# Kernel optimization log

Measured on AMD Instinct MI355X. Metric: run time of the kernel, lower is better.

## Reference

```python
import jax, jax.numpy as jnp
import numpy as np

D_MODEL = 1024
D_QK = 1024
NUM_HEADS = 16
HEAD_DIM = D_QK // NUM_HEADS      # 64
V_DIM = D_MODEL // NUM_HEADS      # 64
B, S = 2, 2048


def setup_inputs() -> dict:
    key = jax.random.key(0)
    ks = jax.random.split(key, 9)
    sc = 0.02
    return {
        "x": jax.random.normal(ks[0], (B, S, D_MODEL), dtype=jnp.float32),
        "Wqk": jax.random.normal(ks[1], (D_MODEL, 2 * D_QK), dtype=jnp.float32) * sc,
        "bqk": jax.random.normal(ks[2], (2 * D_QK,), dtype=jnp.float32) * sc,
        "Wv": jax.random.normal(ks[3], (D_MODEL, D_MODEL), dtype=jnp.float32) * sc,
        "bv": jax.random.normal(ks[4], (D_MODEL,), dtype=jnp.float32) * sc,
        "Wn": jax.random.normal(ks[5], (D_MODEL, NUM_HEADS), dtype=jnp.float32) * sc,
        "bn": jax.random.normal(ks[6], (NUM_HEADS,), dtype=jnp.float32) * sc,
        "Wo": jax.random.normal(ks[7], (D_MODEL, D_MODEL), dtype=jnp.float32) * sc,
        "bo": jax.random.normal(ks[8], (D_MODEL,), dtype=jnp.float32) * sc,
    }


def reference(x, Wqk, bqk, Wv, bv, Wn, bn, Wo, bo):
    b, s, _ = x.shape
    qk = x @ Wqk + bqk                                  # (B,S,2*D_QK)
    v = x @ Wv + bv                                     # (B,S,D_MODEL)
    n = x @ Wn + bn                                     # (B,S,H)

    qk = qk.reshape(b, s, 2, NUM_HEADS, HEAD_DIM)
    q, k = qk[:, :, 0], qk[:, :, 1]                     # (B,S,H,Dh)
    v = v.reshape(b, s, NUM_HEADS, V_DIM)               # (B,S,H,Dv)

    scores = jnp.einsum('bthd,bshd->bhts', q, k)        # (B,H,S,S)
    mask = jnp.tril(jnp.ones((s, s), dtype=scores.dtype))
    n_exp = jnp.exp(jnp.transpose(n, (0, 2, 1)))        # (B,H,S)
    attn = scores * mask / n_exp[:, :, :, None]         # dropout p=0 (eval)

    ctx = jnp.einsum('bhts,bshd->bthd', attn, v)        # (B,S,H,Dv)
    ctx = ctx.reshape(b, s, D_MODEL)
    return ctx @ Wo + bo
```

## Files before the change

kernel.cpp:

```cpp
#include <hip/hip_runtime.h>
#include <hip/hip_bf16.h>

constexpr int Bb   = 2;
constexpr int Ss   = 2048;
constexpr int Dm   = 1024;
constexpr int Hh   = 16;
constexpr int Hd   = 64;
constexpr int Mtot = Bb * Ss;
constexpr int NCH  = Ss / 64;

typedef __bf16 bf16x8 __attribute__((ext_vector_type(8)));
typedef float  f32x4  __attribute__((ext_vector_type(4)));
typedef __attribute__((address_space(1))) unsigned int u32_as1;
typedef __attribute__((address_space(3))) unsigned int u32_as3;

__device__ __forceinline__ void gload_lds16(const void* g, void* l) {
  __builtin_amdgcn_global_load_lds((const u32_as1*)g, (u32_as3*)l, 16, 0, 0);
}

__device__ __forceinline__ unsigned short f2bf(float f) {
  union { float f; unsigned u; } x; x.f = f;
  unsigned r = x.u + 0x7fffu + ((x.u >> 16) & 1u);
  return (unsigned short)(r >> 16);
}

__device__ __forceinline__ float bf2f(unsigned short s) {
  union { unsigned u; float f; } x; x.u = ((unsigned)s) << 16;
  return x.f;
}

__global__ __launch_bounds__(256) void k_prep(
    const float* __restrict__ x, const float* __restrict__ Wn, const float* __restrict__ bn,
    float* __restrict__ invn, unsigned short* __restrict__ xb,
    const float* __restrict__ Wqk, const float* __restrict__ Wv, const float* __restrict__ Wo,
    unsigned short* __restrict__ wprojT, unsigned short* __restrict__ woT) {
  __shared__ __align__(16) char smem[16384];
  int bi = blockIdx.x;
  int tid = threadIdx.x;
  if (bi < 1024) {
    float (*xl)[1024] = (float(*)[1024])smem;
    int w = tid >> 6, lane = tid & 63;
    int row = bi * 4 + w;
    const float4* x4 = (const float4*)(x + (size_t)row * Dm);
    ushort4* xb4 = (ushort4*)(xb + (size_t)row * Dm);
#pragma unroll
    for (int j = 0; j < 4; ++j) {
      float4 v = x4[j * 64 + lane];
      *(float4*)&xl[w][(j * 64 + lane) * 4] = v;
      ushort4 o;
      o.x = f2bf(v.x); o.y = f2bf(v.y); o.z = f2bf(v.z); o.w = f2bf(v.w);
      xb4[j * 64 + lane] = o;
    }
    __syncthreads();
    const float4* Wn4 = (const float4*)Wn;
    f32x4 sum = {0.f, 0.f, 0.f, 0.f};
#pragma unroll 4
    for (int j = 0; j < 64; ++j) {
      float xv = xl[w][j * 16 + (lane >> 2)];
      float4 wv = Wn4[j * 64 + lane];
      sum[0] += xv * wv.x; sum[1] += xv * wv.y; sum[2] += xv * wv.z; sum[3] += xv * wv.w;
    }
#pragma unroll
    for (int m = 4; m < 64; m <<= 1) {
      sum[0] += __shfl_xor(sum[0], m);
      sum[1] += __shfl_xor(sum[1], m);
      sum[2] += __shfl_xor(sum[2], m);
      sum[3] += __shfl_xor(sum[3], m);
    }
    if (lane < 4) {
      int b = row >> 11, s = row & 2047;
#pragma unroll
      for (int e = 0; e < 4; ++e) {
        int h = lane * 4 + e;
        float nv = sum[e] + bn[h];
        invn[((size_t)(b * Hh + h)) * Ss + s] = expf(-nv);
      }
    }
  } else {
    float (*t)[33] = (float(*)[33])smem;
    int ti = bi - 1024;
    const float* W; unsigned short* Wt; int N, n0, k0;
    if (ti < 2048) {
      W = Wqk; Wt = wprojT; N = 2048;
      n0 = (ti & 63) * 32; k0 = (ti >> 6) * 32;
    } else if (ti < 3072) {
      int l = ti - 2048; W = Wv; Wt = wprojT + (size_t)2048 * 1024; N = 1024;
      n0 = (l & 31) * 32; k0 = (l >> 5) * 32;
    } else {
      int l = ti - 3072; W = Wo; Wt = woT; N = 1024;
      n0 = (l & 31) * 32; k0 = (l >> 5) * 32;
    }
    int tx = tid & 31, ty = tid >> 5;
#pragma unroll
    for (int j = 0; j < 32; j += 8)
      t[ty + j][tx] = W[(size_t)(k0 + ty + j) * N + n0 + tx];
    __syncthreads();
#pragma unroll
    for (int j = 0; j < 32; j += 8)
      Wt[(size_t)(n0 + ty + j) * 1024 + k0 + tx] = f2bf(t[tx][ty + j]);
  }
}

__global__ __launch_bounds__(256, 4) void k_gemm_proj(
    const unsigned short* __restrict__ A, const unsigned short* __restrict__ BT,
    const float* __restrict__ bias0, const float* __restrict__ bias1,
    void* __restrict__ out0, void* __restrict__ out1, void* __restrict__ out2,
    void* __restrict__ out3, int M, int N, int K) {
  __shared__ __align__(16) unsigned short As[128 * 64];
  __shared__ __align__(16) unsigned short Bs[128 * 64];
  int tid = threadIdx.x, w = tid >> 6, lane = tid & 63;
  int bid = blockIdx.y * gridDim.x + blockIdx.x;
  int xcd = bid & 7, idx = bid >> 3;
  int m0 = (xcd * 4 + (idx & 3)) * 128;
  int n0 = (idx >> 2) * 128;
  int wm = w >> 1, wn = w & 1;
  f32x4 acc[4][4] = {};

  for (int kt = 0; kt < (K >> 6); ++kt) {
#pragma unroll
    for (int i = 0; i < 4; ++i) {
      int lin = i * 2048 + w * 512 + lane * 8;
      int r = lin >> 6, c = lin & 63;
      gload_lds16(A + (size_t)(m0 + r) * K + kt * 64 + c, As + i * 2048 + w * 512);
    }
#pragma unroll
    for (int i = 0; i < 4; ++i) {
      int lin = i * 2048 + w * 512 + lane * 8;
      int r = lin >> 6, c = lin & 63;
      gload_lds16(BT + (size_t)(n0 + r) * K + kt * 64 + c, Bs + i * 2048 + w * 512);
    }
    __syncthreads();
#pragma unroll
    for (int ks = 0; ks < 2; ++ks) {
      bf16x8 af[4], bfr[4];
#pragma unroll
      for (int mt = 0; mt < 4; ++mt)
        af[mt] = *(const bf16x8*)(As + (wm * 64 + mt * 16 + (lane & 15)) * 64 + ks * 32 + (lane >> 4) * 8);
#pragma unroll
      for (int nt = 0; nt < 4; ++nt)
        bfr[nt] = *(const bf16x8*)(Bs + (wn * 64 + nt * 16 + (lane & 15)) * 64 + ks * 32 + (lane >> 4) * 8);
#pragma unroll
      for (int mt = 0; mt < 4; ++mt)
#pragma unroll
        for (int nt = 0; nt < 4; ++nt)
          acc[mt][nt] = __builtin_amdgcn_mfma_f32_16x16x32_bf16(af[mt], bfr[nt], acc[mt][nt], 0, 0, 0);
    }
    __syncthreads();
  }

#pragma unroll
  for (int mt = 0; mt < 4; ++mt) {
#pragma unroll
    for (int nt = 0; nt < 4; ++nt) {
      int n = n0 + wn * 64 + nt * 16 + (lane & 15);
      int tbase = m0 + wm * 64 + mt * 16 + (lane >> 4) * 4;
      int region = n >> 10;
      int h = (n >> 6) & 15, d = n & 63;
      int b = tbase >> 11, t = tbase & 2047;
      float bb = (region < 2) ? bias0[n] : bias1[n - 2048];
      if (region == 0) {
        unsigned short* qp = (unsigned short*)out0;
#pragma unroll
        for (int r = 0; r < 4; ++r)
          qp[(((size_t)(b * Hh + h)) * Ss + t + r) * Hd + d] = f2bf(acc[mt][nt][r] + bb);
      } else if (region == 1) {
        unsigned short* kp = (unsigned short*)out1;
#pragma unroll
        for (int r = 0; r < 4; ++r)
          kp[(((size_t)(b * Hh + h)) * Ss + t + r) * Hd + d] = f2bf(acc[mt][nt][r] + bb);
        ushort4 o;
        o.x = f2bf(acc[mt][nt][0] + bb);
        o.y = f2bf(acc[mt][nt][1] + bb);
        o.z = f2bf(acc[mt][nt][2] + bb);
        o.w = f2bf(acc[mt][nt][3] + bb);
        *(ushort4*)((unsigned short*)out2 + ((size_t)(b * Hh + h) * Hd + d) * Ss + t) = o;
      } else {
        ushort4 o;
        o.x = f2bf(acc[mt][nt][0] + bb);
        o.y = f2bf(acc[mt][nt][1] + bb);
        o.z = f2bf(acc[mt][nt][2] + bb);
        o.w = f2bf(acc[mt][nt][3] + bb);
        *(ushort4*)((unsigned short*)out3 + ((size_t)(b * Hh + h) * Hd + d) * Ss + t) = o;
      }
    }
  }
}

__global__ __launch_bounds__(256, 3) void k_gemm_o(
    const unsigned short* __restrict__ A, const unsigned short* __restrict__ BT,
    const float* __restrict__ bias, float* __restrict__ out) {
  constexpr int K = 1024, N = 1024;
  __shared__ __align__(16) unsigned short As[2][64 * 64];
  __shared__ __align__(16) unsigned short Bs[2][128 * 64];
  int tid = threadIdx.x, w = tid >> 6, lane = tid & 63;
  int bid = blockIdx.y * gridDim.x + blockIdx.x;
  int xcd = bid & 7, idx = bid >> 3;
  int m0 = (xcd * 8 + (idx & 7)) * 64;
  int n0 = (idx >> 3) * 128;
  int wm = w >> 1, wn = w & 1;
  f32x4 acc[2][4] = {};

  auto STAGE = [&](int kt, int cur) {
#pragma unroll
    for (int i = 0; i < 2; ++i) {
      int lin = i * 2048 + w * 512 + lane * 8;
      int r = lin >> 6, c = lin & 63;
      gload_lds16(A + (size_t)(m0 + r) * K + kt * 64 + c, As[cur] + i * 2048 + w * 512);
    }
#pragma unroll
    for (int i = 0; i < 4; ++i) {
      int lin = i * 2048 + w * 512 + lane * 8;
      int r = lin >> 6, c = lin & 63;
      gload_lds16(BT + (size_t)(n0 + r) * K + kt * 64 + c, Bs[cur] + i * 2048 + w * 512);
    }
  };

  constexpr int NT = K >> 6;
  STAGE(0, 0);
  __syncthreads();
  for (int kt = 0; kt < NT; ++kt) {
    int cur = kt & 1;
    if (kt + 1 < NT) STAGE(kt + 1, cur ^ 1);
#pragma unroll
    for (int ks = 0; ks < 2; ++ks) {
      bf16x8 af[2], bfr[4];
#pragma unroll
      for (int mt = 0; mt < 2; ++mt)
        af[mt] = *(const bf16x8*)(As[cur] + (wm * 32 + mt * 16 + (lane & 15)) * 64 + ks * 32 + (lane >> 4) * 8);
#pragma unroll
      for (int nt = 0; nt < 4; ++nt)
        bfr[nt] = *(const bf16x8*)(Bs[cur] + (wn * 64 + nt * 16 + (lane & 15)) * 64 + ks * 32 + (lane >> 4) * 8);
#pragma unroll
      for (int mt = 0; mt < 2; ++mt)
#pragma unroll
        for (int nt = 0; nt < 4; ++nt)
          acc[mt][nt] = __builtin_amdgcn_mfma_f32_16x16x32_bf16(af[mt], bfr[nt], acc[mt][nt], 0, 0, 0);
    }
    __syncthreads();
  }

#pragma unroll
  for (int mt = 0; mt < 2; ++mt) {
#pragma unroll
    for (int nt = 0; nt < 4; ++nt) {
      int n = n0 + wn * 64 + nt * 16 + (lane & 15);
      int m = m0 + wm * 32 + mt * 16 + (lane >> 4) * 4;
      float bb = bias[n];
#pragma unroll
      for (int r = 0; r < 4; ++r)
        out[(size_t)(m + r) * N + n] = acc[mt][nt][r] + bb;
    }
  }
}

__global__ __launch_bounds__(64) void k_gram(
    const unsigned short* __restrict__ vT, const unsigned short* __restrict__ kT,
    unsigned short* __restrict__ G) {
  int lane = threadIdx.x;
  int j = blockIdx.x, bh = blockIdx.y;
  int t0 = j * 64;
  const unsigned short* vb = vT + (size_t)bh * Hd * Ss;
  const unsigned short* kb = kT + (size_t)bh * Hd * Ss;
  unsigned short* g = G + ((size_t)bh * NCH + j) * 4096;

  bf16x8 af[4][2], bfr[4][2];
#pragma unroll
  for (int mt = 0; mt < 4; ++mt)
#pragma unroll
    for (int ks = 0; ks < 2; ++ks) {
      af[mt][ks]  = *(const bf16x8*)(vb + (size_t)(mt * 16 + (lane & 15)) * Ss + t0 + ks * 32 + (lane >> 4) * 8);
      bfr[mt][ks] = *(const bf16x8*)(kb + (size_t)(mt * 16 + (lane & 15)) * Ss + t0 + ks * 32 + (lane >> 4) * 8);
    }
  f32x4 acc[4][4] = {};
#pragma unroll
  for (int mt = 0; mt < 4; ++mt)
#pragma unroll
    for (int nt = 0; nt < 4; ++nt)
#pragma unroll
      for (int ks = 0; ks < 2; ++ks)
        acc[mt][nt] = __builtin_amdgcn_mfma_f32_16x16x32_bf16(af[mt][ks], bfr[nt][ks], acc[mt][nt], 0, 0, 0);
#pragma unroll
  for (int mt = 0; mt < 4; ++mt)
#pragma unroll
    for (int nt = 0; nt < 4; ++nt)
#pragma unroll
      for (int r = 0; r < 4; ++r)
        g[(mt * 16 + (lane >> 4) * 4 + r) * 64 + nt * 16 + (lane & 15)] = f2bf(acc[mt][nt][r]);
}

__global__ __launch_bounds__(256) void k_prefix(
    const unsigned short* __restrict__ G, unsigned short* __restrict__ Sp) {
  int gidx = blockIdx.x * 256 + threadIdx.x;
  int bh = gidx >> 12, e = gidx & 4095;
  const unsigned short* gp = G + (size_t)bh * NCH * 4096 + e;
  unsigned short* sp = Sp + (size_t)bh * NCH * 4096 + e;
  float acc = 0.f;
#pragma unroll 8
  for (int j = 0; j < NCH; ++j) {
    sp[(size_t)j * 4096] = f2bf(acc);
    acc += bf2f(gp[(size_t)j * 4096]);
  }
}

__global__ __launch_bounds__(256, 6) void k_chunk_attn(
    const unsigned short* __restrict__ q, const unsigned short* __restrict__ k,
    const unsigned short* __restrict__ vT, const unsigned short* __restrict__ Sp,
    const float* __restrict__ invn, unsigned short* __restrict__ ctx) {
  __shared__ __align__(16) unsigned short P[4 * 16 * 64];
  int tid = threadIdx.x, w = tid >> 6, lane = tid & 63;
  int j = blockIdx.x, bh = blockIdx.y;
  int t0 = j * 64;
  const unsigned short* qb = q + (size_t)bh * Ss * Hd;
  const unsigned short* kb = k + (size_t)bh * Ss * Hd;
  const unsigned short* vb = vT + (size_t)bh * Hd * Ss;
  const unsigned short* sp = Sp + ((size_t)bh * NCH + j) * 4096;

  bf16x8 qf[2];
#pragma unroll
  for (int ks = 0; ks < 2; ++ks)
    qf[ks] = *(const bf16x8*)(qb + (size_t)(t0 + w * 16 + (lane & 15)) * Hd + ks * 32 + (lane >> 4) * 8);

  f32x4 acc[4] = {};
#pragma unroll
  for (int nt = 0; nt < 4; ++nt)
#pragma unroll
    for (int ks = 0; ks < 2; ++ks) {
      bf16x8 sf = *(const bf16x8*)(sp + (nt * 16 + (lane & 15)) * 64 + ks * 32 + (lane >> 4) * 8);
      acc[nt] = __builtin_amdgcn_mfma_f32_16x16x32_bf16(qf[ks], sf, acc[nt], 0, 0, 0);
    }

  f32x4 sacc[4] = {};
#pragma unroll
  for (int nt = 0; nt < 4; ++nt)
#pragma unroll
    for (int ks = 0; ks < 2; ++ks) {
      bf16x8 kf = *(const bf16x8*)(kb + (size_t)(t0 + nt * 16 + (lane & 15)) * Hd + ks * 32 + (lane >> 4) * 8);
      sacc[nt] = __builtin_amdgcn_mfma_f32_16x16x32_bf16(qf[ks], kf, sacc[nt], 0, 0, 0);
    }

#pragma unroll
  for (int nt = 0; nt < 4; ++nt)
#pragma unroll
    for (int r = 0; r < 4; ++r) {
      int row = (lane >> 4) * 4 + r;
      int s_local = nt * 16 + (lane & 15);
      float vv = (s_local <= w * 16 + row) ? sacc[nt][r] : 0.f;
      int cb = s_local * 2;
      int byte = w * 2048 + row * 128 + (cb ^ ((row & 7) << 4));
      *(unsigned short*)((char*)P + byte) = f2bf(vv);
    }
  asm volatile("" ::: "memory");

  bf16x8 pf[2];
#pragma unroll
  for (int ks = 0; ks < 2; ++ks) {
    int prow = lane & 15;
    int pcb = (ks * 32 + (lane >> 4) * 8) * 2;
    pf[ks] = *(const bf16x8*)((char*)P + w * 2048 + prow * 128 + (pcb ^ ((prow & 7) << 4)));
  }
#pragma unroll
  for (int dt = 0; dt < 4; ++dt)
#pragma unroll
    for (int ks = 0; ks < 2; ++ks) {
      bf16x8 vf = *(const bf16x8*)(vb + (size_t)(dt * 16 + (lane & 15)) * Ss + t0 + ks * 32 + (lane >> 4) * 8);
      acc[dt] = __builtin_amdgcn_mfma_f32_16x16x32_bf16(pf[ks], vf, acc[dt], 0, 0, 0);
    }

  int b = bh >> 4, h = bh & 15;
  float sc[4];
#pragma unroll
  for (int r = 0; r < 4; ++r)
    sc[r] = invn[(size_t)bh * Ss + t0 + w * 16 + (lane >> 4) * 4 + r];
#pragma unroll
  for (int dt = 0; dt < 4; ++dt)
#pragma unroll
    for (int r = 0; r < 4; ++r) {
      int t = t0 + w * 16 + (lane >> 4) * 4 + r;
      size_t m = (size_t)b * Ss + t;
      ctx[m * Dm + h * Hd + dt * 16 + (lane & 15)] = f2bf(acc[dt][r] * sc[r]);
    }
}

extern "C" void kernel_launch(void* const* d_in, const int* in_sizes, int n_in,
                              void* d_out, int out_size, void* d_ws, size_t ws_size,
                              hipStream_t stream) {
  const float* x   = (const float*)d_in[0];
  const float* Wqk = (const float*)d_in[1];
  const float* bqk = (const float*)d_in[2];
  const float* Wv  = (const float*)d_in[3];
  const float* bv  = (const float*)d_in[4];
  const float* Wn  = (const float*)d_in[5];
  const float* bn  = (const float*)d_in[6];
  const float* Wo  = (const float*)d_in[7];
  const float* bo  = (const float*)d_in[8];

  char* ws = (char*)d_ws;
  size_t off = 0;
  unsigned short* xb    = (unsigned short*)(ws + off); off += (size_t)Mtot * Dm * 2;
  unsigned short* wprojT= (unsigned short*)(ws + off); off += (size_t)3072 * 1024 * 2;
  unsigned short* woT   = (unsigned short*)(ws + off); off += (size_t)1024 * 1024 * 2;
  unsigned short* qbuf  = (unsigned short*)(ws + off); off += (size_t)Bb * Hh * Ss * Hd * 2;
  unsigned short* kbuf  = (unsigned short*)(ws + off); off += (size_t)Bb * Hh * Ss * Hd * 2;
  unsigned short* ktbuf = (unsigned short*)(ws + off); off += (size_t)Bb * Hh * Ss * Hd * 2;
  unsigned short* vbuf  = (unsigned short*)(ws + off); off += (size_t)Bb * Hh * Ss * Hd * 2;
  float* invn           = (float*)(ws + off);          off += (size_t)Bb * Hh * Ss * 4;
  unsigned short* G     = (unsigned short*)(ws + off); off += (size_t)Bb * Hh * NCH * 4096 * 2;
  unsigned short* Sp    = (unsigned short*)(ws + off); off += (size_t)Bb * Hh * NCH * 4096 * 2;
  unsigned short* ctx   = xb;

  k_prep<<<5120, 256, 0, stream>>>(x, Wn, bn, invn, xb, Wqk, Wv, Wo, wprojT, woT);

  k_gemm_proj<<<dim3(3072 / 128, Mtot / 128), 256, 0, stream>>>(
      xb, wprojT, bqk, bv, qbuf, kbuf, ktbuf, vbuf, Mtot, 3072, 1024);

  k_gram<<<dim3(NCH, Bb * Hh), 64, 0, stream>>>(vbuf, ktbuf, G);
  k_prefix<<<(Bb * Hh * 4096) / 256, 256, 0, stream>>>(G, Sp);
  k_chunk_attn<<<dim3(NCH, Bb * Hh), 256, 0, stream>>>(qbuf, kbuf, vbuf, Sp, invn, ctx);

  k_gemm_o<<<dim3(1024 / 128, Mtot / 64), 256, 0, stream>>>(ctx, woT, bo, (float*)d_out);
}
```

Baseline: 104.0 us.

## Rewrite projection GEMM as 256x256 double-buffered 8-wave pipelined kernel

Replaces the 128x128, 256-thread projection GEMM with a 256x256 tile, 512-thread kernel. It double-buffers 128KB of LDS, issues the next k-step's global-to-LDS loads between MFMA groups, and XOR-swizzles the LDS columns to avoid bank conflicts. It also remaps blocks across XCDs and raises MFMA priority with setprio. The goal is to hide global load latency and improve operand reuse, at the cost of fewer, larger blocks (192) and heavier register and LDS pressure.

```diff
diff --git a/kernel.cpp b/kernel.cpp
--- a/kernel.cpp
+++ b/kernel.cpp
@@ -101,59 +101,100 @@
   }
 }
 
-__global__ __launch_bounds__(256, 4) void k_gemm_proj(
+__global__ __launch_bounds__(512, 2) void k_gemm_proj8(
     const unsigned short* __restrict__ A, const unsigned short* __restrict__ BT,
     const float* __restrict__ bias0, const float* __restrict__ bias1,
     void* __restrict__ out0, void* __restrict__ out1, void* __restrict__ out2,
-    void* __restrict__ out3, int M, int N, int K) {
-  __shared__ __align__(16) unsigned short As[128 * 64];
-  __shared__ __align__(16) unsigned short Bs[128 * 64];
+    void* __restrict__ out3) {
+  constexpr int K = 1024, NT = 16;
+  __shared__ __align__(16) char lds[131072];
   int tid = threadIdx.x, w = tid >> 6, lane = tid & 63;
+  int wm = w >> 2, wn = w & 3;
+
   int bid = blockIdx.y * gridDim.x + blockIdx.x;
-  int xcd = bid & 7, idx = bid >> 3;
-  int m0 = (xcd * 4 + (idx & 3)) * 128;
-  int n0 = (idx >> 2) * 128;
-  int wm = w >> 1, wn = w & 1;
-  f32x4 acc[4][4] = {};
-
-  for (int kt = 0; kt < (K >> 6); ++kt) {
-#pragma unroll
-    for (int i = 0; i < 4; ++i) {
-      int lin = i * 2048 + w * 512 + lane * 8;
-      int r = lin >> 6, c = lin & 63;
-      gload_lds16(A + (size_t)(m0 + r) * K + kt * 64 + c, As + i * 2048 + w * 512);
-    }
-#pragma unroll
-    for (int i = 0; i < 4; ++i) {
-      int lin = i * 2048 + w * 512 + lane * 8;
-      int r = lin >> 6, c = lin & 63;
-      gload_lds16(BT + (size_t)(n0 + r) * K + kt * 64 + c, Bs + i * 2048 + w * 512);
-    }
-    __syncthreads();
-#pragma unroll
-    for (int ks = 0; ks < 2; ++ks) {
-      bf16x8 af[4], bfr[4];
-#pragma unroll
-      for (int mt = 0; mt < 4; ++mt)
-        af[mt] = *(const bf16x8*)(As + (wm * 64 + mt * 16 + (lane & 15)) * 64 + ks * 32 + (lane >> 4) * 8);
-#pragma unroll
-      for (int nt = 0; nt < 4; ++nt)
-        bfr[nt] = *(const bf16x8*)(Bs + (wn * 64 + nt * 16 + (lane & 15)) * 64 + ks * 32 + (lane >> 4) * 8);
-#pragma unroll
-      for (int mt = 0; mt < 4; ++mt)
-#pragma unroll
-        for (int nt = 0; nt < 4; ++nt)
-          acc[mt][nt] = __builtin_amdgcn_mfma_f32_16x16x32_bf16(af[mt], bfr[nt], acc[mt][nt], 0, 0, 0);
-    }
-    __syncthreads();
-  }
-
-#pragma unroll
-  for (int mt = 0; mt < 4; ++mt) {
-#pragma unroll
-    for (int nt = 0; nt < 4; ++nt) {
-      int n = n0 + wn * 64 + nt * 16 + (lane & 15);
-      int tbase = m0 + wm * 64 + mt * 16 + (lane >> 4) * 4;
+  int swz = (bid & 7) * 24 + (bid >> 3);
+  int by = swz / 12, bx = swz % 12;
+  int m0 = by * 256, n0 = bx * 256;
+
+  int d0 = w * 1024 + lane * 16;
+  int r0 = d0 >> 6, lc0 = ((d0 & 63) ^ ((r0 & 3) << 4)) >> 1;
+  int r1 = r0 + 128;
+  int cS = ((lane >> 4) << 4) ^ ((lane & 3) << 4);
+  int rA = (lane & 15);
+
+  f32x4 acc[8][4] = {};
+
+  auto STG = [&](int buf, int kt, int ks, int i) {
+    int rr = i ? r1 : r0;
+    int gc = kt * 64 + ks * 32 + lc0;
+    char* db = lds + buf * 65536 + ks * 16384 + i * 8192 + w * 1024;
+    gload_lds16(A  + (size_t)(m0 + rr) * K + gc, db);
+    gload_lds16(BT + (size_t)(n0 + rr) * K + gc, db + 32768);
+  };
+
+  STG(0, 0, 0, 0); STG(0, 0, 0, 1);
+  STG(0, 0, 1, 0); STG(0, 0, 1, 1);
+  asm volatile("s_waitcnt vmcnt(4)" ::: "memory");
+  __builtin_amdgcn_s_barrier();
+  asm volatile("" ::: "memory");
+
+  for (int t = 0; t < NT; ++t) {
+    int buf = t & 1, sb = buf ^ 1;
+    int tn = (t + 1 < NT) ? t + 1 : t;
+    const char* Lb = lds + buf * 65536;
+    bf16x8 af[4], bfr[4];
+
+#pragma unroll
+    for (int ks = 0; ks < 2; ++ks) {
+      const char* La = Lb + ks * 16384;
+      const char* Bv = Lb + 32768 + ks * 16384;
+#pragma unroll
+      for (int nf = 0; nf < 4; ++nf)
+        bfr[nf] = *(const bf16x8*)(Bv + (wn * 64 + nf * 16 + rA) * 64 + cS);
+#pragma unroll
+      for (int mf = 0; mf < 4; ++mf)
+        af[mf] = *(const bf16x8*)(La + (wm * 128 + mf * 16 + rA) * 64 + cS);
+      STG(sb, tn, ks, 0);
+      asm volatile("" ::: "memory");
+      __builtin_amdgcn_s_barrier();
+      __builtin_amdgcn_s_setprio(1);
+#pragma unroll
+      for (int mf = 0; mf < 4; ++mf)
+#pragma unroll
+        for (int nf = 0; nf < 4; ++nf)
+          acc[mf][nf] = __builtin_amdgcn_mfma_f32_16x16x32_bf16(af[mf], bfr[nf], acc[mf][nf], 0, 0, 0);
+      __builtin_amdgcn_s_setprio(0);
+      __builtin_amdgcn_sched_barrier(0);
+      asm volatile("" ::: "memory");
+      __builtin_amdgcn_s_barrier();
+
+#pragma unroll
+      for (int mf = 0; mf < 4; ++mf)
+        af[mf] = *(const bf16x8*)(La + (wm * 128 + (mf + 4) * 16 + rA) * 64 + cS);
+      STG(sb, tn, ks, 1);
+      asm volatile("" ::: "memory");
+      __builtin_amdgcn_s_barrier();
+      __builtin_amdgcn_s_setprio(1);
+#pragma unroll
+      for (int mf = 0; mf < 4; ++mf)
+#pragma unroll
+        for (int nf = 0; nf < 4; ++nf)
+          acc[mf + 4][nf] = __builtin_amdgcn_mfma_f32_16x16x32_bf16(af[mf], bfr[nf], acc[mf + 4][nf], 0, 0, 0);
+      __builtin_amdgcn_s_setprio(0);
+      __builtin_amdgcn_sched_barrier(0);
+      asm volatile("s_waitcnt vmcnt(4)" ::: "memory");
+      __builtin_amdgcn_s_barrier();
+      asm volatile("" ::: "memory");
+    }
+  }
+  asm volatile("s_waitcnt vmcnt(0) lgkmcnt(0)" ::: "memory");
+
+#pragma unroll
+  for (int mf = 0; mf < 8; ++mf) {
+#pragma unroll
+    for (int nf = 0; nf < 4; ++nf) {
+      int n = n0 + wn * 64 + nf * 16 + (lane & 15);
+      int tbase = m0 + wm * 128 + mf * 16 + (lane >> 4) * 4;
       int region = n >> 10;
       int h = (n >> 6) & 15, d = n & 63;
       int b = tbase >> 11, t = tbase & 2047;
@@ -162,24 +203,24 @@
         unsigned short* qp = (unsigned short*)out0;
 #pragma unroll
         for (int r = 0; r < 4; ++r)
-          qp[(((size_t)(b * Hh + h)) * Ss + t + r) * Hd + d] = f2bf(acc[mt][nt][r] + bb);
+          qp[(((size_t)(b * Hh + h)) * Ss + t + r) * Hd + d] = f2bf(acc[mf][nf][r] + bb);
       } else if (region == 1) {
         unsigned short* kp = (unsigned short*)out1;
 #pragma unroll
         for (int r = 0; r < 4; ++r)
-          kp[(((size_t)(b * Hh + h)) * Ss + t + r) * Hd + d] = f2bf(acc[mt][nt][r] + bb);
+          kp[(((size_t)(b * Hh + h)) * Ss + t + r) * Hd + d] = f2bf(acc[mf][nf][r] + bb);
         ushort4 o;
-        o.x = f2bf(acc[mt][nt][0] + bb);
-        o.y = f2bf(acc[mt][nt][1] + bb);
-        o.z = f2bf(acc[mt][nt][2] + bb);
-        o.w = f2bf(acc[mt][nt][3] + bb);
+        o.x = f2bf(acc[mf][nf][0] + bb);
+        o.y = f2bf(acc[mf][nf][1] + bb);
+        o.z = f2bf(acc[mf][nf][2] + bb);
+        o.w = f2bf(acc[mf][nf][3] + bb);
         *(ushort4*)((unsigned short*)out2 + ((size_t)(b * Hh + h) * Hd + d) * Ss + t) = o;
       } else {
         ushort4 o;
-        o.x = f2bf(acc[mt][nt][0] + bb);
-        o.y = f2bf(acc[mt][nt][1] + bb);
-        o.z = f2bf(acc[mt][nt][2] + bb);
-        o.w = f2bf(acc[mt][nt][3] + bb);
+        o.x = f2bf(acc[mf][nf][0] + bb);
+        o.y = f2bf(acc[mf][nf][1] + bb);
+        o.z = f2bf(acc[mf][nf][2] + bb);
+        o.w = f2bf(acc[mf][nf][3] + bb);
         *(ushort4*)((unsigned short*)out3 + ((size_t)(b * Hh + h) * Hd + d) * Ss + t) = o;
       }
     }
@@ -410,8 +451,8 @@
 
   k_prep<<<5120, 256, 0, stream>>>(x, Wn, bn, invn, xb, Wqk, Wv, Wo, wprojT, woT);
 
-  k_gemm_proj<<<dim3(3072 / 128, Mtot / 128), 256, 0, stream>>>(
-      xb, wprojT, bqk, bv, qbuf, kbuf, ktbuf, vbuf, Mtot, 3072, 1024);
+  k_gemm_proj8<<<dim3(3072 / 256, Mtot / 256), 512, 0, stream>>>(
+      xb, wprojT, bqk, bv, qbuf, kbuf, ktbuf, vbuf);
 
   k_gram<<<dim3(NCH, Bb * Hh), 64, 0, stream>>>(vbuf, ktbuf, G);
   k_prefix<<<(Bb * Hh * 4096) / 256, 256, 0, stream>>>(G, Sp);
```

After: 108.0 us. 1.04x slower.
